# Kernel tuning notes

Hardware: AMD Instinct MI355X
Metric: run time of the kernel (lower is better)

## Reference

```python
import jax, jax.numpy as jnp
import numpy as np

HID = 2048
NEXP = 16
BRD = max(64, HID // 8)        # block_router_dim = 256
BATCH, SEQ = 4, 8192
BASE_BS, MAX_BS = 512, 2048
BASE_THR, BASE_BUDGET = 0.6, 0.3


def _adjust(seq_len):
    # mirrors _adjust_parameters_for_length (static: depends only on shape)
    if seq_len <= 4096:
        return BASE_BS, BASE_THR, BASE_BUDGET
    elif seq_len <= 16384:
        return min(1024, MAX_BS), BASE_THR * 1.1, BASE_BUDGET * 0.7
    else:
        scale = min(seq_len / 16384, 4)
        return min(int(BASE_BS * scale), MAX_BS), BASE_THR * 1.2, BASE_BUDGET * (1.0 / scale)


def _layernorm(x, g, b, eps=1e-5):
    m = x.mean(-1, keepdims=True)
    v = ((x - m) ** 2).mean(-1, keepdims=True)
    return (x - m) / jnp.sqrt(v + eps) * g + b


def setup_inputs() -> dict:
    key = jax.random.key(0)
    k = jax.random.split(key, 6)
    return {
        "hidden_states": jax.random.normal(k[0], (BATCH, SEQ, HID), jnp.float32),
        # block_router: Linear(H->256) -> LN -> GELU -> Linear(256->E)
        "bw1": jax.random.normal(k[1], (HID, BRD), jnp.float32) * 0.02,
        "bb1": jnp.zeros((BRD,), jnp.float32),
        "ln_g": jnp.ones((BRD,), jnp.float32),
        "ln_b": jnp.zeros((BRD,), jnp.float32),
        # final block-router layer scaled up so block entropies spread around the
        # 0.66 threshold and both routing branches are exercised
        "bw2": jax.random.normal(k[2], (BRD, NEXP), jnp.float32) * 0.6,
        "bb2": jnp.zeros((NEXP,), jnp.float32),
        # token_router: Linear(H->H/2) -> GELU -> (Dropout: eval/identity) -> Linear(H/2->E)
        "tw1": jax.random.normal(k[3], (HID, HID // 2), jnp.float32) * 0.02,
        "tb1": jnp.zeros((HID // 2,), jnp.float32),
        "tw2": jax.random.normal(k[4], (HID // 2, NEXP), jnp.float32) * 0.02,
        "tb2": jnp.zeros((NEXP,), jnp.float32),
    }


def reference(hidden_states, bw1, bb1, ln_g, ln_b, bw2, bb2, tw1, tb1, tw2, tb2):
    B, S, H = hidden_states.shape
    E = bw2.shape[1]
    bs, thr, budget = _adjust(S)
    assert S % bs == 0, "reference assumes seq_len divisible by block_size"
    N = S // bs
    max_tok = int(S * budget)               # python int (static)
    k_budget = max(1, max_tok // bs)        # blocks_within_budget (static)

    # --- block-level routing ---
    block_repr = hidden_states.reshape(B, N, bs, H).mean(2)          # [B,N,H]
    h = _layernorm(block_repr @ bw1 + bb1, ln_g, ln_b)
    block_logits = jax.nn.gelu(h, approximate=False) @ bw2 + bb2     # [B,N,E]
    block_probs = jax.nn.softmax(block_logits, -1)
    p = block_probs + 1e-10
    entropy = -jnp.sum(p * jnp.log(p), -1) / jnp.log(jnp.float32(E))  # [B,N]

    mask1 = entropy > thr
    total_high = mask1.sum()
    # budget-based threshold adjustment (k-th largest high entropy)
    flat_ent = jnp.where(mask1.ravel(), entropy.ravel(), -jnp.inf)
    kth = jnp.sort(flat_ent)[::-1][k_budget - 1]
    cond = (total_high * bs > max_tok) & (total_high > 0) & (k_budget < total_high)
    mask2 = jnp.where(cond, entropy > kth, mask1)

    # sequential token budget over flattened (batch, block) row-major order
    cum = jnp.cumsum(mask2.ravel().astype(jnp.int32) * bs).reshape(B, N)
    token_flag = mask2 & (cum <= max_tok)            # per-token routing
    block_flag = (~mask1) | (mask2 & ~token_flag)    # block-level routing

    # block weight scatter: argmax one-hot * max prob (detached, torch uses .item())
    bw = jax.lax.stop_gradient(
        jax.nn.one_hot(jnp.argmax(block_probs, -1), E, dtype=block_probs.dtype)
        * jnp.max(block_probs, -1, keepdims=True))   # [B,N,E]

    # token-level routing computed densely, masked (dropout in eval mode = identity)
    th = jax.nn.gelu(hidden_states @ tw1 + tb1, approximate=False)
    token_probs = jax.nn.softmax(th @ tw2 + tb2, -1)  # [B,S,E]

    tf = jnp.repeat(token_flag, bs, axis=1)[..., None]   # [B,S,1]
    bf = jnp.repeat(block_flag, bs, axis=1)[..., None]
    bw_tok = jnp.repeat(bw, bs, axis=1)                  # [B,S,E]
    routing = jnp.where(tf, token_probs, jnp.where(bf, bw_tok, jnp.zeros((), hidden_states.dtype)))

    usage = routing.mean((0, 1))
    target = 1.0 / E
    aux = jnp.sum(target * jnp.log(target / (usage + 1e-10)))
    return routing, aux
```

## Files before the change

### kernel.cpp

```cpp
#include <hip/hip_runtime.h>
#include <math.h>

#define BB 4
#define SS 8192
#define HH 2048
#define EE 16
#define BRD_ 256
#define BSZ 1024
#define NN 8
#define NB 32
#define MAXTOK 1720
#define HHALF 1024
#define TC 16
#define ROWS 64
#define KSP 32
#define KL 64
#define JL 64

typedef __attribute__((ext_vector_type(8))) short bf16x8;
typedef __attribute__((ext_vector_type(4))) float f32x4;
typedef __attribute__((ext_vector_type(4))) float f32x4v;

__device__ inline short f2bf(float f) {
  unsigned u = __builtin_bit_cast(unsigned, f);
  u += 0x7FFFu + ((u >> 16) & 1u);
  return (short)(u >> 16);
}

__device__ inline void wave_flags(const double* __restrict__ ent, int l,
                                  int& flag_out, int& fb_out) {
  const double THR = 0.6 * 1.1;
  double e = (l < NB) ? ent[l] : -INFINITY;
  bool m1 = (l < NB) && (e > THR);
  unsigned long long m1mask = __ballot(m1);
  int th = __popcll(m1mask);
  double sel = m1 ? e : -INFINITY;
  #pragma unroll
  for (int o = 32; o; o >>= 1) sel = fmax(sel, __shfl_xor(sel, o));
  bool m2 = (th >= 2) ? ((l < NB) && (e > sel)) : m1;
  unsigned long long m2mask = __ballot(m2);
  int cum = __popcll(m2mask & ((2ULL << l) - 1ULL)) * BSZ;
  bool tf = m2 && (cum <= MAXTOK);
  bool bf = (l < NB) && ((!m1) || (m2 && !tf));
  flag_out = tf ? 1 : (bf ? 2 : 0);
  unsigned long long tfmask = __ballot(tf);
  fb_out = tfmask ? (__ffsll(tfmask) - 1) : -1;
}

__global__ __launch_bounds__(256) void k_bmean(const float* __restrict__ x,
                                               double* __restrict__ part) {
  int wg = blockIdx.x;
  int bn = wg >> 4, tc = wg & 15;
  int b = bn >> 3, n = bn & 7;
  int tid = threadIdx.x;
  const float* base = x + ((size_t)(b * SS + n * BSZ + tc * ROWS) * HH);
  double a0=0,a1=0,a2=0,a3=0,a4=0,a5=0,a6=0,a7=0;
  #pragma unroll 4
  for (int t = 0; t < ROWS; ++t) {
    const f32x4v* r = (const f32x4v*)(base + (size_t)t * HH);
    f32x4v u = __builtin_nontemporal_load(r + tid);
    f32x4v v = __builtin_nontemporal_load(r + tid + 256);
    a0 += u.x; a1 += u.y; a2 += u.z; a3 += u.w;
    a4 += v.x; a5 += v.y; a6 += v.z; a7 += v.w;
  }
  double* p = part + ((size_t)bn * TC + tc) * HH;
  int hA = tid * 4, hB = 1024 + tid * 4;
  p[hA] = a0; p[hA+1] = a1; p[hA+2] = a2; p[hA+3] = a3;
  p[hB] = a4; p[hB+1] = a5; p[hB+2] = a6; p[hB+3] = a7;
}

__global__ __launch_bounds__(256) void k_g1(const double* __restrict__ part,
    const float* __restrict__ bw1, double* __restrict__ g1part) {
  __shared__ double brs[NB][KL];
  __shared__ float  wsm[KL][JL];
  int bid = blockIdx.x;
  int kq = bid >> 2, jt = bid & 3;
  int k0 = kq * KL, j0 = jt * JL;
  int tid = threadIdx.x;
  #pragma unroll
  for (int i = 0; i < 8; ++i) {
    int e = i * 256 + tid;
    int bn = e >> 6, k = e & 63;
    const double* pp = part + ((size_t)bn * TC) * HH + k0 + k;
    double s = 0;
    #pragma unroll
    for (int tc = 0; tc < TC; ++tc) s += pp[(size_t)tc * HH];
    brs[bn][k] = s * (1.0 / BSZ);
  }
  #pragma unroll
  for (int i = 0; i < 4; ++i) {
    int f = i * 256 + tid;
    int r = f >> 4, c4 = f & 15;
    float4 v = *(const float4*)(bw1 + (size_t)(k0 + r) * BRD_ + j0 + c4 * 4);
    *(float4*)&wsm[r][c4 * 4] = v;
  }
  __syncthreads();
  int j = tid & 63;
  int bh = (tid >> 6) * 8;
  double acc[8];
  #pragma unroll
  for (int r = 0; r < 8; ++r) acc[r] = 0;
  #pragma unroll 8
  for (int k = 0; k < KL; ++k) {
    double wv = (double)wsm[k][j];
    #pragma unroll
    for (int r = 0; r < 8; ++r) acc[r] += brs[bh + r][k] * wv;
  }
  #pragma unroll
  for (int r = 0; r < 8; ++r)
    g1part[((size_t)kq * NB + bh + r) * BRD_ + j0 + j] = acc[r];
}

__global__ __launch_bounds__(256) void k_router2(const double* __restrict__ g1part,
    const float* __restrict__ bb1, const float* __restrict__ lng, const float* __restrict__ lnb,
    const float* __restrict__ bw2, const float* __restrict__ bb2,
    double* __restrict__ ent, float* __restrict__ bwv, int* __restrict__ bwi) {
  __shared__ double tg[BRD_];
  __shared__ double p3[16][EE];
  __shared__ double red[4];
  __shared__ double l2[EE];
  __shared__ double bcast;
  int bn = blockIdx.x, tid = threadIdx.x;

  double a = (double)bb1[tid];
  #pragma unroll
  for (int kq = 0; kq < KSP; ++kq) a += g1part[((size_t)kq * NB + bn) * BRD_ + tid];

  double v = a;
  for (int o = 32; o; o >>= 1) v += __shfl_down(v, o);
  if ((tid & 63) == 0) red[tid >> 6] = v;
  __syncthreads();
  if (tid == 0) bcast = (red[0] + red[1] + red[2] + red[3]) * (1.0 / BRD_);
  __syncthreads();
  double m = bcast;
  double d = a - m;
  v = d * d;
  for (int o = 32; o; o >>= 1) v += __shfl_down(v, o);
  if ((tid & 63) == 0) red[tid >> 6] = v;
  __syncthreads();
  if (tid == 0) bcast = (red[0] + red[1] + red[2] + red[3]) * (1.0 / BRD_);
  __syncthreads();
  double var = bcast;
  double xn = d / sqrt(var + 1e-5) * (double)lng[tid] + (double)lnb[tid];
  tg[tid] = 0.5 * xn * (1.0 + erf(xn * 0.7071067811865476));
  __syncthreads();

  {
    int e = tid & 15, jc = tid >> 4;
    double s = 0;
    const float* w2 = bw2 + (size_t)(jc * 16) * EE + e;
    #pragma unroll
    for (int jj = 0; jj < 16; ++jj) s += tg[jc * 16 + jj] * (double)w2[jj * EE];
    p3[jc][e] = s;
  }
  __syncthreads();
  if (tid < EE) {
    double acc = (double)bb2[tid];
    #pragma unroll
    for (int jc = 0; jc < 16; ++jc) acc += p3[jc][tid];
    l2[tid] = acc;
  }
  __syncthreads();

  if (tid < 64) {
    int e = tid & 15;
    double le = l2[e];
    double mx = le;
    #pragma unroll
    for (int o = 1; o < 16; o <<= 1) mx = fmax(mx, __shfl_xor(mx, o));
    double pe = exp(le - mx);
    double se = pe;
    #pragma unroll
    for (int o = 1; o < 16; o <<= 1) se += __shfl_xor(se, o);
    double pr = pe / se;
    double q = pr + 1e-10;
    double term = -q * log(q);
    double es = term;
    #pragma unroll
    for (int o = 1; o < 16; o <<= 1) es += __shfl_xor(es, o);
    double mp = pr;
    #pragma unroll
    for (int o = 1; o < 16; o <<= 1) mp = fmax(mp, __shfl_xor(mp, o));
    unsigned long long eqm = __ballot((tid < 16) && (pr == mp));
    if (tid == 0) {
      ent[bn] = es / log(16.0);
      bwv[bn] = (float)mp;
      bwi[bn] = __ffsll(eqm) - 1;
    }
  }
}

__global__ __launch_bounds__(256) void k_out(const double* __restrict__ ent,
    const float* __restrict__ bwv, const int* __restrict__ bwi,
    const float* __restrict__ x, const float* __restrict__ tw1, const float* __restrict__ tb1,
    const float* __restrict__ tw2, float* __restrict__ routing, float* __restrict__ lpart) {
  __shared__ int flg_s[NB + 1];
  __shared__ short xs_bf[64][72];
  __shared__ short wsT[64][72];
  __shared__ float ths[64][65];
  int tid = threadIdx.x;
  int bid = blockIdx.x;
  if (tid < 64) {
    int f, fb;
    wave_flags(ent, tid, f, fb);
    if (tid < NB) flg_s[tid] = f;
    if (tid == 0) flg_s[NB] = fb;
  }
  __syncthreads();

  if (bid < 256) {
    int bn = bid >> 3, seg = bid & 7;
    int fl = flg_s[bn];
    if (fl == 1) return;
    int b = bn >> 3, n = bn & 7;
    f32x4v z = {0.f, 0.f, 0.f, 0.f};
    f32x4v val = z;
    int c_hit = -1;
    if (fl == 2) {
      int ai = bwi[bn];
      c_hit = ai >> 2;
      val[ai & 3] = bwv[bn];
    }
    f32x4v* out = (f32x4v*)(routing + ((size_t)(b * SS + n * BSZ + seg * 128) * EE));
    #pragma unroll
    for (int l = 0; l < 2; ++l) {
      int idx = l * 256 + tid;
      int c = idx & 3;
      __builtin_nontemporal_store((c == c_hit) ? val : z, out + idx);
    }
    return;
  }

  int fb = flg_s[NB];
  if (fb < 0) return;
  int b = fb >> 3, n = fb & 7;
  int tb = bid - 256;
  int tg = tb >> 4, nc = tb & 15;
  int t0 = tg * 64, j0 = nc * 64;
  const float* xb = x + ((size_t)(b * SS + n * BSZ + t0) * HH);
  int wv = tid >> 6, lane = tid & 63;
  int wm = (wv >> 1) * 32, wn = (wv & 1) * 32;
  int fr = lane & 15, kg = lane >> 4;
  f32x4 acc00 = {0,0,0,0}, acc01 = {0,0,0,0}, acc10 = {0,0,0,0}, acc11 = {0,0,0,0};

  for (int k0 = 0; k0 < HH; k0 += 64) {
    #pragma unroll
    for (int i = 0; i < 16; ++i) {
      int e = i * 256 + tid; int r = e >> 6, c = e & 63;
      xs_bf[r][c] = f2bf(xb[(size_t)r * HH + k0 + c]);
    }
    #pragma unroll
    for (int i = 0; i < 16; ++i) {
      int e = i * 256 + tid; int r = e >> 6, c = e & 63;
      wsT[c][r] = f2bf(tw1[(size_t)(k0 + r) * HHALF + j0 + c]);
    }
    __syncthreads();
    #pragma unroll
    for (int kc = 0; kc < 64; kc += 32) {
      int ks = kc + kg * 8;
      bf16x8 a0 = *(const bf16x8*)&xs_bf[wm + fr][ks];
      bf16x8 a1 = *(const bf16x8*)&xs_bf[wm + 16 + fr][ks];
      bf16x8 b0 = *(const bf16x8*)&wsT[wn + fr][ks];
      bf16x8 b1 = *(const bf16x8*)&wsT[wn + 16 + fr][ks];
      acc00 = __builtin_amdgcn_mfma_f32_16x16x32_bf16(a0, b0, acc00, 0, 0, 0);
      acc01 = __builtin_amdgcn_mfma_f32_16x16x32_bf16(a0, b1, acc01, 0, 0, 0);
      acc10 = __builtin_amdgcn_mfma_f32_16x16x32_bf16(a1, b0, acc10, 0, 0, 0);
      acc11 = __builtin_amdgcn_mfma_f32_16x16x32_bf16(a1, b1, acc11, 0, 0, 0);
    }
    __syncthreads();
  }
  #pragma unroll
  for (int r = 0; r < 4; ++r) {
    int row0 = wm + kg * 4 + r, row1 = wm + 16 + kg * 4 + r;
    int col0 = wn + fr,         col1 = wn + 16 + fr;
    float v00 = acc00[r] + tb1[j0 + col0];
    float v01 = acc01[r] + tb1[j0 + col1];
    float v10 = acc10[r] + tb1[j0 + col0];
    float v11 = acc11[r] + tb1[j0 + col1];
    ths[row0][col0] = 0.5f * v00 * (1.0f + erff(v00 * 0.70710678f));
    ths[row0][col1] = 0.5f * v01 * (1.0f + erff(v01 * 0.70710678f));
    ths[row1][col0] = 0.5f * v10 * (1.0f + erff(v10 * 0.70710678f));
    ths[row1][col1] = 0.5f * v11 * (1.0f + erff(v11 * 0.70710678f));
  }
  __syncthreads();
  float* lp = lpart + (size_t)nc * (BSZ * EE);
  #pragma unroll
  for (int l = 0; l < 4; ++l) {
    int idx = l * 256 + tid; int t = idx >> 4, e = idx & 15;
    float s = 0;
    #pragma unroll
    for (int jj = 0; jj < 64; ++jj) s += ths[t][jj] * tw2[(size_t)(j0 + jj) * EE + e];
    lp[(t0 + t) * EE + e] = s;
  }
}

__global__ __launch_bounds__(1024) void k_tail(const double* __restrict__ ent,
    const float* __restrict__ lpart, const float* __restrict__ tb2,
    const float* __restrict__ bwv, const int* __restrict__ bwi,
    float* __restrict__ routing, float* __restrict__ outaux) {
  __shared__ int flg_s[NB + 1];
  __shared__ double up[16][EE];
  __shared__ double us[EE];
  int tid = threadIdx.x;
  if (tid < 64) {
    int f, fb;
    wave_flags(ent, tid, f, fb);
    if (tid < NB) flg_s[tid] = f;
    if (tid == 0) flg_s[NB] = fb;
  }
  __syncthreads();
  int fb = flg_s[NB];
  if (fb >= 0) {
    int b = fb >> 3, n = fb & 7;
    int t = tid;
    float l[EE];
    #pragma unroll
    for (int e = 0; e < EE; ++e) {
      float s = tb2[e];
      #pragma unroll
      for (int nc = 0; nc < 16; ++nc) s += lpart[(size_t)nc * (BSZ * EE) + t * EE + e];
      l[e] = s;
    }
    float mx = l[0];
    for (int e = 1; e < EE; ++e) mx = fmaxf(mx, l[e]);
    float se = 0;
    for (int e = 0; e < EE; ++e) { l[e] = expf(l[e] - mx); se += l[e]; }
    float inv = 1.0f / se;
    for (int e = 0; e < EE; ++e) l[e] *= inv;
    float4* orow = (float4*)(routing + ((size_t)(b * SS + n * BSZ + t) * EE));
    orow[0] = make_float4(l[0], l[1], l[2], l[3]);
    orow[1] = make_float4(l[4], l[5], l[6], l[7]);
    orow[2] = make_float4(l[8], l[9], l[10], l[11]);
    orow[3] = make_float4(l[12], l[13], l[14], l[15]);
    int w = tid >> 6;
    for (int e = 0; e < EE; ++e) {
      double v = (double)l[e];
      for (int o = 32; o; o >>= 1) v += __shfl_down(v, o);
      if ((tid & 63) == 0) up[w][e] = v;
    }
  }
  __syncthreads();
  if (tid < EE) {
    double s = 0;
    if (fb >= 0) for (int w = 0; w < 16; ++w) s += up[w][tid];
    for (int i = 0; i < NB; ++i)
      if (flg_s[i] == 2 && bwi[i] == tid) s += (double)BSZ * (double)bwv[i];
    us[tid] = s;
  }
  __syncthreads();
  if (tid == 0) {
    double aux = 0;
    const double target = 1.0 / EE;
    for (int e = 0; e < EE; ++e) {
      double u = us[e] / (double)(BB * SS);
      aux += target * log(target / (u + 1e-10));
    }
    *outaux = (float)aux;
  }
}

extern "C" void kernel_launch(void* const* d_in, const int* in_sizes, int n_in,
                              void* d_out, int out_size, void* d_ws, size_t ws_size,
                              hipStream_t stream) {
  const float* x   = (const float*)d_in[0];
  const float* bw1 = (const float*)d_in[1];
  const float* bb1 = (const float*)d_in[2];
  const float* lng = (const float*)d_in[3];
  const float* lnb = (const float*)d_in[4];
  const float* bw2 = (const float*)d_in[5];
  const float* bb2 = (const float*)d_in[6];
  const float* tw1 = (const float*)d_in[7];
  const float* tb1 = (const float*)d_in[8];
  const float* tw2 = (const float*)d_in[9];
  const float* tb2 = (const float*)d_in[10];
  float* routing = (float*)d_out;
  float* outaux = routing + (size_t)BB * SS * EE;

  char* w = (char*)d_ws;
  size_t off = 0;
  double* part  = (double*)(w + off); off += (size_t)NB * TC * HH * 8;
  double* g1p   = (double*)(w + off); off += (size_t)KSP * NB * BRD_ * 8;
  float*  lpart = (float*) (w + off); off += 16 * (size_t)BSZ * EE * 4;
  double* ent   = (double*)(w + off); off += NB * 8;
  float*  bwv   = (float*) (w + off); off += 256;
  int*    bwi   = (int*)   (w + off); off += 256;

  hipLaunchKernelGGL(k_bmean,   dim3(NB * TC), dim3(256),  0, stream, x, part);
  hipLaunchKernelGGL(k_g1,      dim3(128),     dim3(256),  0, stream, part, bw1, g1p);
  hipLaunchKernelGGL(k_router2, dim3(NB),      dim3(256),  0, stream, g1p,
                     bb1, lng, lnb, bw2, bb2, ent, bwv, bwi);
  hipLaunchKernelGGL(k_out,     dim3(512),     dim3(256),  0, stream, ent, bwv, bwi,
                     x, tw1, tb1, tw2, routing, lpart);
  hipLaunchKernelGGL(k_tail,    dim3(1),       dim3(1024), 0, stream, ent, lpart, tb2,
                     bwv, bwi, routing, outaux);
}
```

Before: 76.78 us.

## Fuse block-mean and first router GEMV into one hidden-slice kernel

The block-mean reduction and the first block-router linear layer are merged into one kernel. Each workgroup now owns a 128-wide hidden slice of one block, reduces all 1024 rows of that slice, and multiplies the slice mean by the matching rows of bw1. This removes the 2 MB double partial-sum buffer, one kernel launch, and the reread of those partials. The cost is narrower float2 loads with a stride of HH between rows, which may coalesce worse than the previous full-row float4 nontemporal loads, and a different floating-point summation order.

```diff
diff --git a/kernel.cpp b/kernel.cpp
--- a/kernel.cpp
+++ b/kernel.cpp
@@ -11,11 +11,8 @@
 #define NB 32
 #define MAXTOK 1720
 #define HHALF 1024
-#define TC 16
-#define ROWS 64
-#define KSP 32
-#define KL 64
-#define JL 64
+#define HSLC 16
+#define HSW 128
 
 typedef __attribute__((ext_vector_type(8))) short bf16x8;
 typedef __attribute__((ext_vector_type(4))) float f32x4;
@@ -47,68 +44,43 @@
   fb_out = tfmask ? (__ffsll(tfmask) - 1) : -1;
 }
 
-__global__ __launch_bounds__(256) void k_bmean(const float* __restrict__ x,
-                                               double* __restrict__ part) {
+__global__ __launch_bounds__(256) void k_meang1(const float* __restrict__ x,
+    const float* __restrict__ bw1, double* __restrict__ g1p) {
+  __shared__ double mq[4][HSW];
+  __shared__ double mean[HSW];
   int wg = blockIdx.x;
-  int bn = wg >> 4, tc = wg & 15;
+  int bn = wg >> 4, hc = wg & 15;
   int b = bn >> 3, n = bn & 7;
   int tid = threadIdx.x;
-  const float* base = x + ((size_t)(b * SS + n * BSZ + tc * ROWS) * HH);
-  double a0=0,a1=0,a2=0,a3=0,a4=0,a5=0,a6=0,a7=0;
-  #pragma unroll 4
-  for (int t = 0; t < ROWS; ++t) {
-    const f32x4v* r = (const f32x4v*)(base + (size_t)t * HH);
-    f32x4v u = __builtin_nontemporal_load(r + tid);
-    f32x4v v = __builtin_nontemporal_load(r + tid + 256);
-    a0 += u.x; a1 += u.y; a2 += u.z; a3 += u.w;
-    a4 += v.x; a5 += v.y; a6 += v.z; a7 += v.w;
-  }
-  double* p = part + ((size_t)bn * TC + tc) * HH;
-  int hA = tid * 4, hB = 1024 + tid * 4;
-  p[hA] = a0; p[hA+1] = a1; p[hA+2] = a2; p[hA+3] = a3;
-  p[hB] = a4; p[hB+1] = a5; p[hB+2] = a6; p[hB+3] = a7;
-}
-
-__global__ __launch_bounds__(256) void k_g1(const double* __restrict__ part,
-    const float* __restrict__ bw1, double* __restrict__ g1part) {
-  __shared__ double brs[NB][KL];
-  __shared__ float  wsm[KL][JL];
-  int bid = blockIdx.x;
-  int kq = bid >> 2, jt = bid & 3;
-  int k0 = kq * KL, j0 = jt * JL;
-  int tid = threadIdx.x;
-  #pragma unroll
-  for (int i = 0; i < 8; ++i) {
-    int e = i * 256 + tid;
-    int bn = e >> 6, k = e & 63;
-    const double* pp = part + ((size_t)bn * TC) * HH + k0 + k;
-    double s = 0;
-    #pragma unroll
-    for (int tc = 0; tc < TC; ++tc) s += pp[(size_t)tc * HH];
-    brs[bn][k] = s * (1.0 / BSZ);
-  }
-  #pragma unroll
-  for (int i = 0; i < 4; ++i) {
-    int f = i * 256 + tid;
-    int r = f >> 4, c4 = f & 15;
-    float4 v = *(const float4*)(bw1 + (size_t)(k0 + r) * BRD_ + j0 + c4 * 4);
-    *(float4*)&wsm[r][c4 * 4] = v;
-  }
-  __syncthreads();
-  int j = tid & 63;
-  int bh = (tid >> 6) * 8;
-  double acc[8];
-  #pragma unroll
-  for (int r = 0; r < 8; ++r) acc[r] = 0;
+  int rq = tid >> 6, lane = tid & 63;
+
+  const float2* p = (const float2*)(x + ((size_t)(b * SS + n * BSZ + rq * 256) * HH) + hc * HSW);
+  double a0 = 0, a1 = 0, a2 = 0, a3 = 0;
   #pragma unroll 8
-  for (int k = 0; k < KL; ++k) {
-    double wv = (double)wsm[k][j];
-    #pragma unroll
-    for (int r = 0; r < 8; ++r) acc[r] += brs[bh + r][k] * wv;
-  }
-  #pragma unroll
-  for (int r = 0; r < 8; ++r)
-    g1part[((size_t)kq * NB + bh + r) * BRD_ + j0 + j] = acc[r];
+  for (int rr = 0; rr < 256; rr += 2) {
+    float2 v0 = p[(size_t)rr * 1024 + lane];
+    float2 v1 = p[(size_t)(rr + 1) * 1024 + lane];
+    a0 += v0.x; a1 += v0.y;
+    a2 += v1.x; a3 += v1.y;
+  }
+  mq[rq][lane * 2]     = a0 + a2;
+  mq[rq][lane * 2 + 1] = a1 + a3;
+  __syncthreads();
+  if (tid < HSW)
+    mean[tid] = (mq[0][tid] + mq[1][tid] + mq[2][tid] + mq[3][tid]) * (1.0 / BSZ);
+  __syncthreads();
+
+  int j = tid;
+  const float* wp = bw1 + (size_t)(hc * HSW) * BRD_ + j;
+  double c0 = 0, c1 = 0, c2 = 0, c3 = 0;
+  #pragma unroll 16
+  for (int k = 0; k < HSW; k += 4) {
+    c0 += mean[k]     * (double)wp[(size_t)k * BRD_];
+    c1 += mean[k + 1] * (double)wp[(size_t)(k + 1) * BRD_];
+    c2 += mean[k + 2] * (double)wp[(size_t)(k + 2) * BRD_];
+    c3 += mean[k + 3] * (double)wp[(size_t)(k + 3) * BRD_];
+  }
+  g1p[((size_t)hc * NB + bn) * BRD_ + j] = (c0 + c1) + (c2 + c3);
 }
 
 __global__ __launch_bounds__(256) void k_router2(const double* __restrict__ g1part,
@@ -124,7 +96,7 @@
 
   double a = (double)bb1[tid];
   #pragma unroll
-  for (int kq = 0; kq < KSP; ++kq) a += g1part[((size_t)kq * NB + bn) * BRD_ + tid];
+  for (int hc = 0; hc < HSLC; ++hc) a += g1part[((size_t)hc * NB + bn) * BRD_ + tid];
 
   double v = a;
   for (int o = 32; o; o >>= 1) v += __shfl_down(v, o);
@@ -378,19 +350,17 @@
 
   char* w = (char*)d_ws;
   size_t off = 0;
-  double* part  = (double*)(w + off); off += (size_t)NB * TC * HH * 8;
-  double* g1p   = (double*)(w + off); off += (size_t)KSP * NB * BRD_ * 8;
+  double* g1p   = (double*)(w + off); off += (size_t)HSLC * NB * BRD_ * 8;
   float*  lpart = (float*) (w + off); off += 16 * (size_t)BSZ * EE * 4;
   double* ent   = (double*)(w + off); off += NB * 8;
   float*  bwv   = (float*) (w + off); off += 256;
   int*    bwi   = (int*)   (w + off); off += 256;
 
-  hipLaunchKernelGGL(k_bmean,   dim3(NB * TC), dim3(256),  0, stream, x, part);
-  hipLaunchKernelGGL(k_g1,      dim3(128),     dim3(256),  0, stream, part, bw1, g1p);
-  hipLaunchKernelGGL(k_router2, dim3(NB),      dim3(256),  0, stream, g1p,
+  hipLaunchKernelGGL(k_meang1,  dim3(NB * HSLC), dim3(256),  0, stream, x, bw1, g1p);
+  hipLaunchKernelGGL(k_router2, dim3(NB),        dim3(256),  0, stream, g1p,
                      bb1, lng, lnb, bw2, bb2, ent, bwv, bwi);
-  hipLaunchKernelGGL(k_out,     dim3(512),     dim3(256),  0, stream, ent, bwv, bwi,
+  hipLaunchKernelGGL(k_out,     dim3(512),       dim3(256),  0, stream, ent, bwv, bwi,
                      x, tw1, tb1, tw2, routing, lpart);
-  hipLaunchKernelGGL(k_tail,    dim3(1),       dim3(1024), 0, stream, ent, lpart, tb2,
+  hipLaunchKernelGGL(k_tail,    dim3(1),         dim3(1024), 0, stream, ent, lpart, tb2,
                      bwv, bwi, routing, outaux);
 }
```

Result: faster. 62.09 us (-19.1%).
